# Kernel tuning notes

Hardware: AMD Instinct MI355X
Metric: run time of the kernel (lower is better)

Reference implementation:

```python
import jax, jax.numpy as jnp
import numpy as np

N_NODES = 50000
N_EDGES = 800000
NFEAT = 128
NHID = 64
NLAYER = 3
BN_EPS = 1e-5


def _bn(h, gamma, beta):
    # BatchNorm1d, training-mode batch statistics (biased variance)
    mu = jnp.mean(h, axis=0)
    var = jnp.mean((h - mu) ** 2, axis=0)
    return gamma * (h - mu) * jax.lax.rsqrt(var + BN_EPS) + beta


def setup_inputs() -> dict:
    key = jax.random.key(0)
    ks = jax.random.split(key, 8)
    x = jax.random.normal(ks[0], (N_NODES, NFEAT), dtype=jnp.float32)
    edge_index = jax.random.randint(ks[1], (2, N_EDGES), 0, N_NODES, dtype=jnp.int64)
    # transform: Linear(nfeat, nhid) with bias, then BN
    W_t = jax.random.normal(ks[2], (NFEAT, NHID), dtype=jnp.float32) / np.sqrt(NFEAT)
    b_t = jnp.zeros((NHID,), dtype=jnp.float32)
    g_t = jnp.ones((NHID,), dtype=jnp.float32)
    bb_t = jnp.zeros((NHID,), dtype=jnp.float32)
    # per-layer GIN MLPs (bias=False) and BN affine params, stacked over layers
    W1 = jax.random.normal(ks[3], (NLAYER, NHID, NHID), dtype=jnp.float32) / np.sqrt(NHID)
    W2 = jax.random.normal(ks[4], (NLAYER, NHID, NHID), dtype=jnp.float32) / np.sqrt(NHID)
    gamma = jnp.ones((NLAYER, NHID), dtype=jnp.float32)
    beta = jnp.zeros((NLAYER, NHID), dtype=jnp.float32)
    return {"x": x, "edge_index": edge_index, "W_t": W_t, "b_t": b_t,
            "g_t": g_t, "bb_t": bb_t, "W1": W1, "W2": W2,
            "gamma": gamma, "beta": beta}


def reference(x, edge_index, W_t, b_t, g_t, bb_t, W1, W2, gamma, beta):
    src, dst = edge_index[0], edge_index[1]
    # input transform: Linear + BN
    h = _bn(x @ W_t + b_t, g_t, bb_t)
    for i in range(NLAYER):
        # dropout p=0 -> identity
        # GINConv (eps=0): (1+eps)*h + sum_{j->i} h_j, then 2-layer MLP
        agg = h + jax.ops.segment_sum(h[src], dst, num_segments=N_NODES)
        h = jax.nn.relu(agg @ W1[i]) @ W2[i]
        h = jax.nn.relu(h)
        h = _bn(h, gamma[i], beta[i])
    # per-graph boolean-mask split is a pure partition of rows; return full matrix
    return h
```

## Files before the change

kernel.cpp:

```cpp
#include <hip/hip_runtime.h>

#define NND 50000
#define NED 800000
#define NF  128
#define NH  64
#define BN_EPS 1e-5
#define NCOPY 8
#define SCB  256
#define NSB  ((NND + SCB - 1) / SCB)
#define XNODES (NND / 8)
#define FCH  196
#define NT   782
#define PGRID (FCH * 8)
#define NE4  (NED / 4)

#define WS_HB     0
#define WS_AGG    6400000
#define WS_STATS  12800000
#define WS_DEG    (WS_STATS + 4*NCOPY*128*4)
#define WS_OFFS   (WS_DEG + NND*4)
#define WS_CUR    (WS_OFFS + (NND+4)*4)
#define WS_PARTS  (WS_CUR + NND*4)
#define WS_ESRC   (WS_PARTS + 256*4)

__device__ __forceinline__ unsigned bfrn(float x) {
    unsigned u = __float_as_uint(x);
    return (u + 0x7fffu + ((u >> 16) & 1u)) >> 16;
}
__device__ __forceinline__ unsigned pk(float lo, float hi) {
    return bfrn(lo) | (bfrn(hi) << 16);
}
__device__ __forceinline__ float ulo(unsigned u) { return __uint_as_float(u << 16); }
__device__ __forceinline__ float uhi(unsigned u) { return __uint_as_float(u & 0xffff0000u); }
__device__ __forceinline__ void upadd(unsigned u, float& lo, float& hi) {
    lo += ulo(u); hi += uhi(u);
}

__device__ __forceinline__ void bn_derive(const float* __restrict__ st, int c,
                                          const float* __restrict__ g,
                                          const float* __restrict__ b,
                                          float& sc, float& sh) {
    float sum = 0.f, ssq = 0.f;
#pragma unroll
    for (int cp = 0; cp < NCOPY; ++cp) {
        sum += st[cp * 128 + c];
        ssq += st[cp * 128 + 64 + c];
    }
    double mu  = (double)sum / (double)NND;
    double var = (double)ssq / (double)NND - mu * mu;
    if (var < 0.0) var = 0.0;
    double rs = 1.0 / sqrt(var + BN_EPS);
    double scd = (double)g[c] * rs;
    sc = (float)scd;
    sh = (float)((double)b[c] - mu * scd);
}

__global__ __launch_bounds__(256) void k_dtf(const int* __restrict__ dst,
                                             int* __restrict__ deg,
                                             const float* __restrict__ x,
                                             const float* __restrict__ Wt,
                                             const float* __restrict__ bt,
                                             unsigned* __restrict__ hB,
                                             float* __restrict__ stats) {
    __shared__ __align__(16) unsigned Wlu[NF * NH / 2];
    __shared__ __align__(16) float sT[64 * 68];
    int tid = threadIdx.x;

    if (blockIdx.x >= NT) {
        int dbid = blockIdx.x - NT;
        int xcd = dbid & 7;
        int chunk = dbid >> 3;
        int lo = xcd * XNODES;
        const int4* d4 = (const int4*)dst;
        int4 d[4];
#pragma unroll
        for (int r = 0; r < 4; ++r) {
            int i = chunk * 1024 + r * 256 + tid;
            int ii = i < NE4 ? i : NE4 - 1;
            d[r] = d4[ii];
            if (i >= NE4) d[r] = make_int4(-1, -1, -1, -1);
        }
#pragma unroll
        for (int r = 0; r < 4; ++r) {
            if ((unsigned)(d[r].x - lo) < XNODES) atomicAdd(&deg[d[r].x], 1);
            if ((unsigned)(d[r].y - lo) < XNODES) atomicAdd(&deg[d[r].y], 1);
            if ((unsigned)(d[r].z - lo) < XNODES) atomicAdd(&deg[d[r].z], 1);
            if ((unsigned)(d[r].w - lo) < XNODES) atomicAdd(&deg[d[r].w], 1);
        }
        return;
    }

    int tile = blockIdx.x;
    int base = tile * 64;
    const float4* x4 = (const float4*)x;

#pragma unroll
    for (int r = 0; r < 8; ++r) {
        int i4 = r * 256 + tid;
        float4 w = ((const float4*)Wt)[i4];
        uint2 wp; wp.x = pk(w.x, w.y); wp.y = pk(w.z, w.w);
        ((uint2*)Wlu)[i4] = wp;
    }

    int wave = tid >> 6, lane = tid & 63;
    int ti = lane & 7, tj = lane >> 3;
    int cw = wave * 32 + tj * 4;

    float acc[8][4];
#pragma unroll
    for (int i = 0; i < 8; ++i)
#pragma unroll
        for (int j = 0; j < 4; ++j) acc[i][j] = 0.f;

    for (int ch = 0; ch < 2; ++ch) {
        __syncthreads();
        float4 pf[4];
#pragma unroll
        for (int s = 0; s < 4; ++s) {
            int flat = s * 256 + tid;
            int nl = flat >> 4, q = flat & 15;
            pf[s] = make_float4(0.f, 0.f, 0.f, 0.f);
            if (base + nl < NND) pf[s] = x4[(size_t)(base + nl) * 32 + ch * 16 + q];
        }
#pragma unroll
        for (int s = 0; s < 4; ++s) {
            int flat = s * 256 + tid;
            int nl = flat >> 4, q = flat & 15;
            sT[(q * 4 + 0) * 68 + nl] = pf[s].x;
            sT[(q * 4 + 1) * 68 + nl] = pf[s].y;
            sT[(q * 4 + 2) * 68 + nl] = pf[s].z;
            sT[(q * 4 + 3) * 68 + nl] = pf[s].w;
        }
        __syncthreads();
        if (tid < 128) {
#pragma unroll 4
            for (int k = 0; k < 64; ++k) {
                const float* ap = &sT[k * 68 + ti * 8];
                float4 alo = *(const float4*)ap;
                float4 ahi = *(const float4*)(ap + 4);
                uint2 wu = *(const uint2*)&Wlu[(ch * 64 + k) * 32 + (cw >> 1)];
                float a8[8] = {alo.x, alo.y, alo.z, alo.w, ahi.x, ahi.y, ahi.z, ahi.w};
                float w4[4] = {ulo(wu.x), uhi(wu.x), ulo(wu.y), uhi(wu.y)};
#pragma unroll
                for (int i = 0; i < 8; ++i)
#pragma unroll
                    for (int j = 0; j < 4; ++j) acc[i][j] += a8[i] * w4[j];
            }
        }
    }
    if (tid >= 128) return;

    float4 bv = *(const float4*)&bt[cw];
    float bj[4] = {bv.x, bv.y, bv.z, bv.w};

    float s4[4] = {0.f, 0.f, 0.f, 0.f}, q4[4] = {0.f, 0.f, 0.f, 0.f};
    uint2* hB2 = (uint2*)hB;
#pragma unroll
    for (int i = 0; i < 8; ++i) {
        int n = base + ti * 8 + i;
        if (n < NND) {
            float o[4];
#pragma unroll
            for (int j = 0; j < 4; ++j) {
                o[j] = acc[i][j] + bj[j];
                s4[j] += o[j];
                q4[j] += o[j] * o[j];
            }
            uint2 ov; ov.x = pk(o[0], o[1]); ov.y = pk(o[2], o[3]);
            hB2[(size_t)n * 16 + wave * 8 + tj] = ov;
        }
    }
#pragma unroll
    for (int m = 1; m < 8; m <<= 1) {
#pragma unroll
        for (int j = 0; j < 4; ++j) {
            s4[j] += __shfl_xor(s4[j], m);
            q4[j] += __shfl_xor(q4[j], m);
        }
    }
    if (ti == 0) {
        int slot = (tile & (NCOPY - 1)) * 128;
#pragma unroll
        for (int j = 0; j < 4; ++j) {
            atomicAdd(&stats[slot + cw + j], s4[j]);
            atomicAdd(&stats[slot + 64 + cw + j], q4[j]);
        }
    }
}

__global__ __launch_bounds__(256) void k_fill(const int* __restrict__ src,
                                              const int* __restrict__ dst,
                                              int* __restrict__ cur,
                                              int* __restrict__ esrc) {
    int xcd = blockIdx.x & 7;
    int chunk = blockIdx.x >> 3;
    int lo = xcd * XNODES;
    const int4* d4 = (const int4*)dst;
    const int4* s4 = (const int4*)src;
    int4 d[4], s[4];
#pragma unroll
    for (int r = 0; r < 4; ++r) {
        int i = chunk * 1024 + r * 256 + threadIdx.x;
        int ii = i < NE4 ? i : NE4 - 1;
        d[r] = d4[ii];
        s[r] = s4[ii];
        if (i >= NE4) d[r] = make_int4(-1, -1, -1, -1);
    }
#pragma unroll
    for (int r = 0; r < 4; ++r) {
        if ((unsigned)(d[r].x - lo) < XNODES) esrc[atomicAdd(&cur[d[r].x], 1)] = s[r].x;
        if ((unsigned)(d[r].y - lo) < XNODES) esrc[atomicAdd(&cur[d[r].y], 1)] = s[r].y;
        if ((unsigned)(d[r].z - lo) < XNODES) esrc[atomicAdd(&cur[d[r].z], 1)] = s[r].z;
        if ((unsigned)(d[r].w - lo) < XNODES) esrc[atomicAdd(&cur[d[r].w], 1)] = s[r].w;
    }
}

__global__ __launch_bounds__(SCB) void k_part(const int* __restrict__ deg,
                                              int* __restrict__ offs,
                                              int* __restrict__ parts) {
    __shared__ int sd[SCB];
    int t = threadIdx.x;
    int i = blockIdx.x * SCB + t;
    int v = (i < NND) ? deg[i] : 0;
    sd[t] = v;
    __syncthreads();
#pragma unroll
    for (int off = 1; off < SCB; off <<= 1) {
        int u = (t >= off) ? sd[t - off] : 0;
        __syncthreads();
        sd[t] += u;
        __syncthreads();
    }
    if (i < NND) offs[i] = sd[t] - v;
    if (t == SCB - 1) parts[blockIdx.x] = sd[t];
}

__global__ __launch_bounds__(256) void k_apply(int* __restrict__ offs,
                                               const int* __restrict__ parts,
                                               int* __restrict__ cur) {
    __shared__ int sd[256];
    int t = threadIdx.x;
    int v = (t < NSB) ? parts[t] : 0;
    sd[t] = v;
    __syncthreads();
#pragma unroll
    for (int off = 1; off < 256; off <<= 1) {
        int u = (t >= off) ? sd[t - off] : 0;
        __syncthreads();
        sd[t] += u;
        __syncthreads();
    }
    int c = blockIdx.x;
    int add = sd[c] - parts[c];
    int i = blockIdx.x * 256 + t;
    if (i < NND) {
        int o = offs[i] + add;
        offs[i] = o;
        cur[i] = o;
    }
    if (i == NND) offs[NND] = NED;
}

__global__ __launch_bounds__(256) void k_agg(const uint4* __restrict__ hB4,
                                             uint4* __restrict__ aggB4,
                                             const float* __restrict__ stats,
                                             const float* __restrict__ g,
                                             const float* __restrict__ b,
                                             const int* __restrict__ offs,
                                             const int* __restrict__ esrc) {
    int tid  = threadIdx.x;
    int lane = tid & 63;
    int wv   = tid >> 6;
    int n = blockIdx.x * 4 + wv;
    int q = lane & 7;
    int r = lane >> 3;

    float scl, shl;
    bn_derive(stats, lane, g, b, scl, shl);

    int e0 = offs[n], e1 = offs[n + 1];
    int deg = e1 - e0;

    float a[8];
#pragma unroll
    for (int i = 0; i < 8; ++i) a[i] = 0.f;

    if (r == 0) {
        uint4 u = hB4[(size_t)n * 8 + q];
        upadd(u.x, a[0], a[1]); upadd(u.y, a[2], a[3]);
        upadd(u.z, a[4], a[5]); upadd(u.w, a[6], a[7]);
    }

    for (int bb = e0; bb < e1; bb += 64) {
        int m = e1 - bb; if (m > 64) m = 64;
        int idx = (lane < m) ? esrc[bb + lane] : 0;
        int ng = (m + 7) >> 3;
        uint4 u[8];
#pragma unroll
        for (int gI = 0; gI < 8; ++gI) {
            if (gI < ng) {
                int e = gI * 8 + r;
                int j = __shfl(idx, e & 63);
                u[gI] = make_uint4(0u, 0u, 0u, 0u);
                if (e < m) u[gI] = hB4[(size_t)j * 8 + q];
            }
        }
#pragma unroll
        for (int gI = 0; gI < 8; ++gI) {
            if (gI < ng) {
                upadd(u[gI].x, a[0], a[1]); upadd(u[gI].y, a[2], a[3]);
                upadd(u[gI].z, a[4], a[5]); upadd(u[gI].w, a[6], a[7]);
            }
        }
    }

#pragma unroll
    for (int msk = 8; msk <= 32; msk <<= 1)
#pragma unroll
        for (int i = 0; i < 8; ++i) a[i] += __shfl_xor(a[i], msk);

    float sc8[8], sh8[8];
#pragma unroll
    for (int j = 0; j < 8; ++j) {
        sc8[j] = __shfl(scl, q * 8 + j);
        sh8[j] = __shfl(shl, q * 8 + j);
    }

    if (r == 0) {
        float dn = (float)(deg + 1);
        float o[8];
#pragma unroll
        for (int j = 0; j < 8; ++j) o[j] = sc8[j] * a[j] + dn * sh8[j];
        uint4 ov;
        ov.x = pk(o[0], o[1]); ov.y = pk(o[2], o[3]);
        ov.z = pk(o[4], o[5]); ov.w = pk(o[6], o[7]);
        aggB4[(size_t)n * 8 + q] = ov;
    }
}

__global__ __launch_bounds__(128) void k_mlp(const uint4* __restrict__ aggB4,
                                             float* __restrict__ outF,
                                             unsigned* __restrict__ hBo,
                                             float* __restrict__ stats,
                                             const float* __restrict__ W1,
                                             const float* __restrict__ W2) {
    __shared__ __align__(16) float W1l[NH * NH];
    __shared__ __align__(16) float W2l[NH * NH];
    __shared__ __align__(16) float sT[64 * 68];
    int tid  = threadIdx.x;
    int wave = tid >> 6, lane = tid & 63;
    int ti = lane & 7, tj = lane >> 3;
    int tile = blockIdx.x;
    int base = tile * 64;
    int cw = wave * 32 + tj * 4;

#pragma unroll
    for (int r = 0; r < 8; ++r) {
        int i4 = r * 128 + tid;
        ((float4*)W1l)[i4] = ((const float4*)W1)[i4];
        ((float4*)W2l)[i4] = ((const float4*)W2)[i4];
    }
#pragma unroll
    for (int s = 0; s < 4; ++s) {
        int i4 = s * 128 + tid;
        int nl = i4 >> 3, q = i4 & 7;
        uint4 u = make_uint4(0u, 0u, 0u, 0u);
        if (base + nl < NND) u = aggB4[(size_t)(base + nl) * 8 + q];
        sT[(q * 8 + 0) * 68 + nl] = ulo(u.x);
        sT[(q * 8 + 1) * 68 + nl] = uhi(u.x);
        sT[(q * 8 + 2) * 68 + nl] = ulo(u.y);
        sT[(q * 8 + 3) * 68 + nl] = uhi(u.y);
        sT[(q * 8 + 4) * 68 + nl] = ulo(u.z);
        sT[(q * 8 + 5) * 68 + nl] = uhi(u.z);
        sT[(q * 8 + 6) * 68 + nl] = ulo(u.w);
        sT[(q * 8 + 7) * 68 + nl] = uhi(u.w);
    }
    __syncthreads();

    float a1[8][4];
#pragma unroll
    for (int i = 0; i < 8; ++i)
#pragma unroll
        for (int j = 0; j < 4; ++j) a1[i][j] = 0.f;
#pragma unroll 4
    for (int k = 0; k < 64; ++k) {
        const float* ap = &sT[k * 68 + ti * 8];
        float4 alo = *(const float4*)ap;
        float4 ahi = *(const float4*)(ap + 4);
        float4 wv  = *(const float4*)&W1l[k * NH + cw];
        float a8[8] = {alo.x, alo.y, alo.z, alo.w, ahi.x, ahi.y, ahi.z, ahi.w};
        float w4[4] = {wv.x, wv.y, wv.z, wv.w};
#pragma unroll
        for (int i = 0; i < 8; ++i)
#pragma unroll
            for (int j = 0; j < 4; ++j) a1[i][j] += a8[i] * w4[j];
    }
#pragma unroll
    for (int i = 0; i < 8; ++i)
#pragma unroll
        for (int j = 0; j < 4; ++j) a1[i][j] = fmaxf(a1[i][j], 0.f);

    __syncthreads();
#pragma unroll
    for (int j = 0; j < 4; ++j) {
        float* p = &sT[(cw + j) * 68 + ti * 8];
        float4 lo = {a1[0][j], a1[1][j], a1[2][j], a1[3][j]};
        float4 hi = {a1[4][j], a1[5][j], a1[6][j], a1[7][j]};
        *(float4*)p = lo;
        *(float4*)(p + 4) = hi;
    }
    __syncthreads();

    float a2[8][4];
#pragma unroll
    for (int i = 0; i < 8; ++i)
#pragma unroll
        for (int j = 0; j < 4; ++j) a2[i][j] = 0.f;
#pragma unroll 4
    for (int k = 0; k < 64; ++k) {
        const float* ap = &sT[k * 68 + ti * 8];
        float4 alo = *(const float4*)ap;
        float4 ahi = *(const float4*)(ap + 4);
        float4 wv  = *(const float4*)&W2l[k * NH + cw];
        float a8[8] = {alo.x, alo.y, alo.z, alo.w, ahi.x, ahi.y, ahi.z, ahi.w};
        float w4[4] = {wv.x, wv.y, wv.z, wv.w};
#pragma unroll
        for (int i = 0; i < 8; ++i)
#pragma unroll
            for (int j = 0; j < 4; ++j) a2[i][j] += a8[i] * w4[j];
    }

    float s4[4] = {0.f, 0.f, 0.f, 0.f}, q4[4] = {0.f, 0.f, 0.f, 0.f};
    uint2* hBo2 = (uint2*)hBo;
#pragma unroll
    for (int i = 0; i < 8; ++i) {
        int n = base + ti * 8 + i;
        if (n < NND) {
            float o[4];
#pragma unroll
            for (int j = 0; j < 4; ++j) {
                o[j] = fmaxf(a2[i][j], 0.f);
                s4[j] += o[j];
                q4[j] += o[j] * o[j];
            }
            if (outF) *(float4*)&outF[(size_t)n * NH + cw] = *(float4*)&o[0];
            if (hBo) {
                uint2 ov; ov.x = pk(o[0], o[1]); ov.y = pk(o[2], o[3]);
                hBo2[(size_t)n * 16 + wave * 8 + tj] = ov;
            }
        }
    }
#pragma unroll
    for (int m = 1; m < 8; m <<= 1) {
#pragma unroll
        for (int j = 0; j < 4; ++j) {
            s4[j] += __shfl_xor(s4[j], m);
            q4[j] += __shfl_xor(q4[j], m);
        }
    }
    if (ti == 0) {
        int slot = (tile & (NCOPY - 1)) * 128;
#pragma unroll
        for (int j = 0; j < 4; ++j) {
            atomicAdd(&stats[slot + cw + j], s4[j]);
            atomicAdd(&stats[slot + 64 + cw + j], q4[j]);
        }
    }
}

__global__ __launch_bounds__(256) void k_bnout(float* __restrict__ h,
                                               const float* __restrict__ stats,
                                               const float* __restrict__ g,
                                               const float* __restrict__ b) {
    __shared__ float sl[128];
    int tid = threadIdx.x;
    if (tid < 64) {
        float sc, sh;
        bn_derive(stats, tid, g, b, sc, sh);
        sl[tid]      = sc;
        sl[64 + tid] = sh;
    }
    __syncthreads();
    int i4 = blockIdx.x * 256 + tid;
    if (i4 < NND * NH / 4) {
        int cg = i4 & 15;
        float4 v   = ((float4*)h)[i4];
        float4 scv = *(float4*)&sl[cg * 4];
        float4 shv = *(float4*)&sl[64 + cg * 4];
        v.x = v.x * scv.x + shv.x;
        v.y = v.y * scv.y + shv.y;
        v.z = v.z * scv.z + shv.z;
        v.w = v.w * scv.w + shv.w;
        ((float4*)h)[i4] = v;
    }
}

extern "C" void kernel_launch(void* const* d_in, const int* in_sizes, int n_in,
                              void* d_out, int out_size, void* d_ws, size_t ws_size,
                              hipStream_t stream) {
    const float* x     = (const float*)d_in[0];
    const int*   ei    = (const int*)d_in[1];
    const float* Wt    = (const float*)d_in[2];
    const float* bt    = (const float*)d_in[3];
    const float* gt    = (const float*)d_in[4];
    const float* bbt   = (const float*)d_in[5];
    const float* W1    = (const float*)d_in[6];
    const float* W2    = (const float*)d_in[7];
    const float* gamma = (const float*)d_in[8];
    const float* beta  = (const float*)d_in[9];
    float* out = (float*)d_out;

    char* ws = (char*)d_ws;
    unsigned* hB    = (unsigned*)(ws + WS_HB);
    unsigned* aggB  = (unsigned*)(ws + WS_AGG);
    float*    stats = (float*)(ws + WS_STATS);
    int*      deg   = (int*)(ws + WS_DEG);
    int*      offs  = (int*)(ws + WS_OFFS);
    int*      cur   = (int*)(ws + WS_CUR);
    int*      parts = (int*)(ws + WS_PARTS);
    int*      esrc  = (int*)(ws + WS_ESRC);

    float* st0 = stats;
    float* st1 = stats + NCOPY * 128;
    float* st2 = stats + 2 * NCOPY * 128;
    float* st3 = stats + 3 * NCOPY * 128;

    const int* srcv = ei;
    const int* dstv = ei + NED;

    hipMemsetAsync(stats, 0, 4 * NCOPY * 128 * 4 + NND * 4, stream);

    k_dtf<<<NT + PGRID, 256, 0, stream>>>(dstv, deg, x, Wt, bt, hB, st0);
    k_part<<<NSB, SCB, 0, stream>>>(deg, offs, parts);
    k_apply<<<NSB, 256, 0, stream>>>(offs, parts, cur);
    k_fill<<<PGRID, 256, 0, stream>>>(srcv, dstv, cur, esrc);

    const int NB = NND / 4;

    k_agg<<<NB, 256, 0, stream>>>((const uint4*)hB, (uint4*)aggB, st0, gt, bbt, offs, esrc);
    k_mlp<<<NT, 128, 0, stream>>>((const uint4*)aggB, nullptr, hB, st1, W1, W2);

    k_agg<<<NB, 256, 0, stream>>>((const uint4*)hB, (uint4*)aggB, st1, gamma, beta, offs, esrc);
    k_mlp<<<NT, 128, 0, stream>>>((const uint4*)aggB, nullptr, hB, st2, W1 + 4096, W2 + 4096);

    k_agg<<<NB, 256, 0, stream>>>((const uint4*)hB, (uint4*)aggB, st2, gamma + 64, beta + 64, offs, esrc);
    k_mlp<<<NT, 128, 0, stream>>>((const uint4*)aggB, out, nullptr, st3, W1 + 8192, W2 + 8192);

    k_bnout<<<(NND * NH / 4 + 255) / 256, 256, 0, stream>>>(out, st3, gamma + 128, beta + 128);
}
```

Measured before the change: 311.3 us.

## Partition each node's CSR neighbor list by source half for gather locality

Counts, per destination, how many in-edges come from sources in the lower half of the node range. Each node's edge slots are split into a low-source segment and a high-source segment through two fill cursors. The aggregation kernel walks the low segment and then the high segment. The aim is better cache locality in the bf16 feature gathers, since concurrent waves tend to touch the same half of the feature table. The cost is an extra atomic degree counter, an extra cursor array, and a second gather loop with more partial tail batches per node.

```diff
diff --git a/kernel.cpp b/kernel.cpp
--- a/kernel.cpp
+++ b/kernel.cpp
@@ -13,14 +13,17 @@
 #define NT   782
 #define PGRID (FCH * 8)
 #define NE4  (NED / 4)
+#define NLOW (NND / 2)
 
 #define WS_HB     0
 #define WS_AGG    6400000
 #define WS_STATS  12800000
 #define WS_DEG    (WS_STATS + 4*NCOPY*128*4)
-#define WS_OFFS   (WS_DEG + NND*4)
+#define WS_LDEG   (WS_DEG + NND*4)
+#define WS_OFFS   (WS_LDEG + NND*4)
 #define WS_CUR    (WS_OFFS + (NND+4)*4)
-#define WS_PARTS  (WS_CUR + NND*4)
+#define WS_CURB   (WS_CUR + NND*4)
+#define WS_PARTS  (WS_CURB + NND*4)
 #define WS_ESRC   (WS_PARTS + 256*4)
 
 __device__ __forceinline__ unsigned bfrn(float x) {
@@ -55,8 +58,38 @@
     sh = (float)((double)b[c] - mu * scd);
 }
 
-__global__ __launch_bounds__(256) void k_dtf(const int* __restrict__ dst,
+__device__ __forceinline__ void gather_range(const uint4* __restrict__ hB4,
+                                             const int* __restrict__ esrc,
+                                             int from, int to,
+                                             int lane, int q, int r, float a[8]) {
+    for (int bb = from; bb < to; bb += 64) {
+        int m = to - bb; if (m > 64) m = 64;
+        int idx = (lane < m) ? esrc[bb + lane] : 0;
+        int ng = (m + 7) >> 3;
+        uint4 u[8];
+#pragma unroll
+        for (int gI = 0; gI < 8; ++gI) {
+            if (gI < ng) {
+                int e = gI * 8 + r;
+                int j = __shfl(idx, e & 63);
+                u[gI] = make_uint4(0u, 0u, 0u, 0u);
+                if (e < m) u[gI] = hB4[(size_t)j * 8 + q];
+            }
+        }
+#pragma unroll
+        for (int gI = 0; gI < 8; ++gI) {
+            if (gI < ng) {
+                upadd(u[gI].x, a[0], a[1]); upadd(u[gI].y, a[2], a[3]);
+                upadd(u[gI].z, a[4], a[5]); upadd(u[gI].w, a[6], a[7]);
+            }
+        }
+    }
+}
+
+__global__ __launch_bounds__(256) void k_dtf(const int* __restrict__ src,
+                                             const int* __restrict__ dst,
                                              int* __restrict__ deg,
+                                             int* __restrict__ ldeg,
                                              const float* __restrict__ x,
                                              const float* __restrict__ Wt,
                                              const float* __restrict__ bt,
@@ -72,20 +105,34 @@
         int chunk = dbid >> 3;
         int lo = xcd * XNODES;
         const int4* d4 = (const int4*)dst;
-        int4 d[4];
+        const int4* s4 = (const int4*)src;
+        int4 d[4], s[4];
 #pragma unroll
         for (int r = 0; r < 4; ++r) {
             int i = chunk * 1024 + r * 256 + tid;
             int ii = i < NE4 ? i : NE4 - 1;
             d[r] = d4[ii];
+            s[r] = s4[ii];
             if (i >= NE4) d[r] = make_int4(-1, -1, -1, -1);
         }
 #pragma unroll
         for (int r = 0; r < 4; ++r) {
-            if ((unsigned)(d[r].x - lo) < XNODES) atomicAdd(&deg[d[r].x], 1);
-            if ((unsigned)(d[r].y - lo) < XNODES) atomicAdd(&deg[d[r].y], 1);
-            if ((unsigned)(d[r].z - lo) < XNODES) atomicAdd(&deg[d[r].z], 1);
-            if ((unsigned)(d[r].w - lo) < XNODES) atomicAdd(&deg[d[r].w], 1);
+            if ((unsigned)(d[r].x - lo) < XNODES) {
+                atomicAdd(&deg[d[r].x], 1);
+                if ((unsigned)s[r].x < NLOW) atomicAdd(&ldeg[d[r].x], 1);
+            }
+            if ((unsigned)(d[r].y - lo) < XNODES) {
+                atomicAdd(&deg[d[r].y], 1);
+                if ((unsigned)s[r].y < NLOW) atomicAdd(&ldeg[d[r].y], 1);
+            }
+            if ((unsigned)(d[r].z - lo) < XNODES) {
+                atomicAdd(&deg[d[r].z], 1);
+                if ((unsigned)s[r].z < NLOW) atomicAdd(&ldeg[d[r].z], 1);
+            }
+            if ((unsigned)(d[r].w - lo) < XNODES) {
+                atomicAdd(&deg[d[r].w], 1);
+                if ((unsigned)s[r].w < NLOW) atomicAdd(&ldeg[d[r].w], 1);
+            }
         }
         return;
     }
@@ -190,7 +237,8 @@
 
 __global__ __launch_bounds__(256) void k_fill(const int* __restrict__ src,
                                               const int* __restrict__ dst,
-                                              int* __restrict__ cur,
+                                              int* __restrict__ curA,
+                                              int* __restrict__ curB,
                                               int* __restrict__ esrc) {
     int xcd = blockIdx.x & 7;
     int chunk = blockIdx.x >> 3;
@@ -208,10 +256,22 @@
     }
 #pragma unroll
     for (int r = 0; r < 4; ++r) {
-        if ((unsigned)(d[r].x - lo) < XNODES) esrc[atomicAdd(&cur[d[r].x], 1)] = s[r].x;
-        if ((unsigned)(d[r].y - lo) < XNODES) esrc[atomicAdd(&cur[d[r].y], 1)] = s[r].y;
-        if ((unsigned)(d[r].z - lo) < XNODES) esrc[atomicAdd(&cur[d[r].z], 1)] = s[r].z;
-        if ((unsigned)(d[r].w - lo) < XNODES) esrc[atomicAdd(&cur[d[r].w], 1)] = s[r].w;
+        if ((unsigned)(d[r].x - lo) < XNODES) {
+            int* c = ((unsigned)s[r].x < NLOW) ? curA : curB;
+            esrc[atomicAdd(&c[d[r].x], 1)] = s[r].x;
+        }
+        if ((unsigned)(d[r].y - lo) < XNODES) {
+            int* c = ((unsigned)s[r].y < NLOW) ? curA : curB;
+            esrc[atomicAdd(&c[d[r].y], 1)] = s[r].y;
+        }
+        if ((unsigned)(d[r].z - lo) < XNODES) {
+            int* c = ((unsigned)s[r].z < NLOW) ? curA : curB;
+            esrc[atomicAdd(&c[d[r].z], 1)] = s[r].z;
+        }
+        if ((unsigned)(d[r].w - lo) < XNODES) {
+            int* c = ((unsigned)s[r].w < NLOW) ? curA : curB;
+            esrc[atomicAdd(&c[d[r].w], 1)] = s[r].w;
+        }
     }
 }
 
@@ -237,7 +297,9 @@
 
 __global__ __launch_bounds__(256) void k_apply(int* __restrict__ offs,
                                                const int* __restrict__ parts,
-                                               int* __restrict__ cur) {
+                                               const int* __restrict__ ldeg,
+                                               int* __restrict__ curA,
+                                               int* __restrict__ curB) {
     __shared__ int sd[256];
     int t = threadIdx.x;
     int v = (t < NSB) ? parts[t] : 0;
@@ -256,7 +318,8 @@
     if (i < NND) {
         int o = offs[i] + add;
         offs[i] = o;
-        cur[i] = o;
+        curA[i] = o;
+        curB[i] = o + ldeg[i];
     }
     if (i == NND) offs[NND] = NED;
 }
@@ -267,6 +330,7 @@
                                              const float* __restrict__ g,
                                              const float* __restrict__ b,
                                              const int* __restrict__ offs,
+                                             const int* __restrict__ ldeg,
                                              const int* __restrict__ esrc) {
     int tid  = threadIdx.x;
     int lane = tid & 63;
@@ -278,8 +342,9 @@
     float scl, shl;
     bn_derive(stats, lane, g, b, scl, shl);
 
-    int e0 = offs[n], e1 = offs[n + 1];
-    int deg = e1 - e0;
+    int e0 = offs[n], e2 = offs[n + 1];
+    int e1 = e0 + ldeg[n];
+    int deg = e2 - e0;
 
     float a[8];
 #pragma unroll
@@ -291,28 +356,8 @@
         upadd(u.z, a[4], a[5]); upadd(u.w, a[6], a[7]);
     }
 
-    for (int bb = e0; bb < e1; bb += 64) {
-        int m = e1 - bb; if (m > 64) m = 64;
-        int idx = (lane < m) ? esrc[bb + lane] : 0;
-        int ng = (m + 7) >> 3;
-        uint4 u[8];
-#pragma unroll
-        for (int gI = 0; gI < 8; ++gI) {
-            if (gI < ng) {
-                int e = gI * 8 + r;
-                int j = __shfl(idx, e & 63);
-                u[gI] = make_uint4(0u, 0u, 0u, 0u);
-                if (e < m) u[gI] = hB4[(size_t)j * 8 + q];
-            }
-        }
-#pragma unroll
-        for (int gI = 0; gI < 8; ++gI) {
-            if (gI < ng) {
-                upadd(u[gI].x, a[0], a[1]); upadd(u[gI].y, a[2], a[3]);
-                upadd(u[gI].z, a[4], a[5]); upadd(u[gI].w, a[6], a[7]);
-            }
-        }
-    }
+    gather_range(hB4, esrc, e0, e1, lane, q, r, a);
+    gather_range(hB4, esrc, e1, e2, lane, q, r, a);
 
 #pragma unroll
     for (int msk = 8; msk <= 32; msk <<= 1)
@@ -515,8 +560,10 @@
     unsigned* aggB  = (unsigned*)(ws + WS_AGG);
     float*    stats = (float*)(ws + WS_STATS);
     int*      deg   = (int*)(ws + WS_DEG);
+    int*      ldeg  = (int*)(ws + WS_LDEG);
     int*      offs  = (int*)(ws + WS_OFFS);
-    int*      cur   = (int*)(ws + WS_CUR);
+    int*      curA  = (int*)(ws + WS_CUR);
+    int*      curB  = (int*)(ws + WS_CURB);
     int*      parts = (int*)(ws + WS_PARTS);
     int*      esrc  = (int*)(ws + WS_ESRC);
 
@@ -528,22 +575,22 @@
     const int* srcv = ei;
     const int* dstv = ei + NED;
 
-    hipMemsetAsync(stats, 0, 4 * NCOPY * 128 * 4 + NND * 4, stream);
-
-    k_dtf<<<NT + PGRID, 256, 0, stream>>>(dstv, deg, x, Wt, bt, hB, st0);
+    hipMemsetAsync(stats, 0, 4 * NCOPY * 128 * 4 + 2 * NND * 4, stream);
+
+    k_dtf<<<NT + PGRID, 256, 0, stream>>>(srcv, dstv, deg, ldeg, x, Wt, bt, hB, st0);
     k_part<<<NSB, SCB, 0, stream>>>(deg, offs, parts);
-    k_apply<<<NSB, 256, 0, stream>>>(offs, parts, cur);
-    k_fill<<<PGRID, 256, 0, stream>>>(srcv, dstv, cur, esrc);
+    k_apply<<<NSB, 256, 0, stream>>>(offs, parts, ldeg, curA, curB);
+    k_fill<<<PGRID, 256, 0, stream>>>(srcv, dstv, curA, curB, esrc);
 
     const int NB = NND / 4;
 
-    k_agg<<<NB, 256, 0, stream>>>((const uint4*)hB, (uint4*)aggB, st0, gt, bbt, offs, esrc);
+    k_agg<<<NB, 256, 0, stream>>>((const uint4*)hB, (uint4*)aggB, st0, gt, bbt, offs, ldeg, esrc);
     k_mlp<<<NT, 128, 0, stream>>>((const uint4*)aggB, nullptr, hB, st1, W1, W2);
 
-    k_agg<<<NB, 256, 0, stream>>>((const uint4*)hB, (uint4*)aggB, st1, gamma, beta, offs, esrc);
+    k_agg<<<NB, 256, 0, stream>>>((const uint4*)hB, (uint4*)aggB, st1, gamma, beta, offs, ldeg, esrc);
     k_mlp<<<NT, 128, 0, stream>>>((const uint4*)aggB, nullptr, hB, st2, W1 + 4096, W2 + 4096);
 
-    k_agg<<<NB, 256, 0, stream>>>((const uint4*)hB, (uint4*)aggB, st2, gamma + 64, beta + 64, offs, esrc);
+    k_agg<<<NB, 256, 0, stream>>>((const uint4*)hB, (uint4*)aggB, st2, gamma + 64, beta + 64, offs, ldeg, esrc);
     k_mlp<<<NT, 128, 0, stream>>>((const uint4*)aggB, out, nullptr, st3, W1 + 8192, W2 + 8192);
 
     k_bnout<<<(NND * NH / 4 + 255) / 256, 256, 0, stream>>>(out, st3, gamma + 128, beta + 128);
```

Result: slower. 347.9 us (+11.7%).

## Split bf16 feature storage into two column-half planes and aggregate per half

Applied to the files above, without the earlier changes.

Node features are stored as two separate planes of 32 columns each instead of interleaved 64-column rows, and the gather-aggregation kernel is launched twice, once per half. Each pass's random gather working set becomes half the size (50000×64B), which improves L2 hit rate for irregular neighbor reads. The cost is twice the launches, re-reading the edge index and offsets in both passes, and narrower 64-byte gathers per edge.

```diff
diff --git a/kernel.cpp b/kernel.cpp
--- a/kernel.cpp
+++ b/kernel.cpp
@@ -167,7 +167,7 @@
                 q4[j] += o[j] * o[j];
             }
             uint2 ov; ov.x = pk(o[0], o[1]); ov.y = pk(o[2], o[3]);
-            hB2[(size_t)n * 16 + wave * 8 + tj] = ov;
+            hB2[((size_t)wave * NND + n) * 8 + tj] = ov;
         }
     }
 #pragma unroll
@@ -267,16 +267,18 @@
                                              const float* __restrict__ g,
                                              const float* __restrict__ b,
                                              const int* __restrict__ offs,
-                                             const int* __restrict__ esrc) {
+                                             const int* __restrict__ esrc,
+                                             int half) {
     int tid  = threadIdx.x;
     int lane = tid & 63;
     int wv   = tid >> 6;
     int n = blockIdx.x * 4 + wv;
-    int q = lane & 7;
-    int r = lane >> 3;
+    int q = lane & 3;
+    int r = lane >> 2;
+    size_t hbase = (size_t)half * NND;
 
     float scl, shl;
-    bn_derive(stats, lane, g, b, scl, shl);
+    bn_derive(stats, half * 32 + (lane & 31), g, b, scl, shl);
 
     int e0 = offs[n], e1 = offs[n + 1];
     int deg = e1 - e0;
@@ -286,7 +288,7 @@
     for (int i = 0; i < 8; ++i) a[i] = 0.f;
 
     if (r == 0) {
-        uint4 u = hB4[(size_t)n * 8 + q];
+        uint4 u = hB4[(hbase + n) * 4 + q];
         upadd(u.x, a[0], a[1]); upadd(u.y, a[2], a[3]);
         upadd(u.z, a[4], a[5]); upadd(u.w, a[6], a[7]);
     }
@@ -294,19 +296,19 @@
     for (int bb = e0; bb < e1; bb += 64) {
         int m = e1 - bb; if (m > 64) m = 64;
         int idx = (lane < m) ? esrc[bb + lane] : 0;
-        int ng = (m + 7) >> 3;
-        uint4 u[8];
-#pragma unroll
-        for (int gI = 0; gI < 8; ++gI) {
+        int ng = (m + 15) >> 4;
+        uint4 u[4];
+#pragma unroll
+        for (int gI = 0; gI < 4; ++gI) {
             if (gI < ng) {
-                int e = gI * 8 + r;
+                int e = gI * 16 + r;
                 int j = __shfl(idx, e & 63);
                 u[gI] = make_uint4(0u, 0u, 0u, 0u);
-                if (e < m) u[gI] = hB4[(size_t)j * 8 + q];
+                if (e < m) u[gI] = hB4[(hbase + j) * 4 + q];
             }
         }
 #pragma unroll
-        for (int gI = 0; gI < 8; ++gI) {
+        for (int gI = 0; gI < 4; ++gI) {
             if (gI < ng) {
                 upadd(u[gI].x, a[0], a[1]); upadd(u[gI].y, a[2], a[3]);
                 upadd(u[gI].z, a[4], a[5]); upadd(u[gI].w, a[6], a[7]);
@@ -315,7 +317,7 @@
     }
 
 #pragma unroll
-    for (int msk = 8; msk <= 32; msk <<= 1)
+    for (int msk = 4; msk <= 32; msk <<= 1)
 #pragma unroll
         for (int i = 0; i < 8; ++i) a[i] += __shfl_xor(a[i], msk);
 
@@ -334,7 +336,7 @@
         uint4 ov;
         ov.x = pk(o[0], o[1]); ov.y = pk(o[2], o[3]);
         ov.z = pk(o[4], o[5]); ov.w = pk(o[6], o[7]);
-        aggB4[(size_t)n * 8 + q] = ov;
+        aggB4[(hbase + n) * 4 + q] = ov;
     }
 }
 
@@ -363,17 +365,19 @@
 #pragma unroll
     for (int s = 0; s < 4; ++s) {
         int i4 = s * 128 + tid;
-        int nl = i4 >> 3, q = i4 & 7;
+        int nl = i4 >> 3, z = i4 & 7;
+        int h = z >> 2, qq = z & 3;
         uint4 u = make_uint4(0u, 0u, 0u, 0u);
-        if (base + nl < NND) u = aggB4[(size_t)(base + nl) * 8 + q];
-        sT[(q * 8 + 0) * 68 + nl] = ulo(u.x);
-        sT[(q * 8 + 1) * 68 + nl] = uhi(u.x);
-        sT[(q * 8 + 2) * 68 + nl] = ulo(u.y);
-        sT[(q * 8 + 3) * 68 + nl] = uhi(u.y);
-        sT[(q * 8 + 4) * 68 + nl] = ulo(u.z);
-        sT[(q * 8 + 5) * 68 + nl] = uhi(u.z);
-        sT[(q * 8 + 6) * 68 + nl] = ulo(u.w);
-        sT[(q * 8 + 7) * 68 + nl] = uhi(u.w);
+        if (base + nl < NND) u = aggB4[((size_t)h * NND + base + nl) * 4 + qq];
+        int c0 = h * 32 + qq * 8;
+        sT[(c0 + 0) * 68 + nl] = ulo(u.x);
+        sT[(c0 + 1) * 68 + nl] = uhi(u.x);
+        sT[(c0 + 2) * 68 + nl] = ulo(u.y);
+        sT[(c0 + 3) * 68 + nl] = uhi(u.y);
+        sT[(c0 + 4) * 68 + nl] = ulo(u.z);
+        sT[(c0 + 5) * 68 + nl] = uhi(u.z);
+        sT[(c0 + 6) * 68 + nl] = ulo(u.w);
+        sT[(c0 + 7) * 68 + nl] = uhi(u.w);
     }
     __syncthreads();
 
@@ -446,7 +450,7 @@
             if (outF) *(float4*)&outF[(size_t)n * NH + cw] = *(float4*)&o[0];
             if (hBo) {
                 uint2 ov; ov.x = pk(o[0], o[1]); ov.y = pk(o[2], o[3]);
-                hBo2[(size_t)n * 16 + wave * 8 + tj] = ov;
+                hBo2[((size_t)wave * NND + n) * 8 + tj] = ov;
             }
         }
     }
@@ -537,13 +541,16 @@
 
     const int NB = NND / 4;
 
-    k_agg<<<NB, 256, 0, stream>>>((const uint4*)hB, (uint4*)aggB, st0, gt, bbt, offs, esrc);
+    k_agg<<<NB, 256, 0, stream>>>((const uint4*)hB, (uint4*)aggB, st0, gt, bbt, offs, esrc, 0);
+    k_agg<<<NB, 256, 0, stream>>>((const uint4*)hB, (uint4*)aggB, st0, gt, bbt, offs, esrc, 1);
     k_mlp<<<NT, 128, 0, stream>>>((const uint4*)aggB, nullptr, hB, st1, W1, W2);
 
-    k_agg<<<NB, 256, 0, stream>>>((const uint4*)hB, (uint4*)aggB, st1, gamma, beta, offs, esrc);
+    k_agg<<<NB, 256, 0, stream>>>((const uint4*)hB, (uint4*)aggB, st1, gamma, beta, offs, esrc, 0);
+    k_agg<<<NB, 256, 0, stream>>>((const uint4*)hB, (uint4*)aggB, st1, gamma, beta, offs, esrc, 1);
     k_mlp<<<NT, 128, 0, stream>>>((const uint4*)aggB, nullptr, hB, st2, W1 + 4096, W2 + 4096);
 
-    k_agg<<<NB, 256, 0, stream>>>((const uint4*)hB, (uint4*)aggB, st2, gamma + 64, beta + 64, offs, esrc);
+    k_agg<<<NB, 256, 0, stream>>>((const uint4*)hB, (uint4*)aggB, st2, gamma + 64, beta + 64, offs, esrc, 0);
+    k_agg<<<NB, 256, 0, stream>>>((const uint4*)hB, (uint4*)aggB, st2, gamma + 64, beta + 64, offs, esrc, 1);
     k_mlp<<<NT, 128, 0, stream>>>((const uint4*)aggB, out, nullptr, st3, W1 + 8192, W2 + 8192);
 
     k_bnout<<<(NND * NH / 4 + 255) / 256, 256, 0, stream>>>(out, st3, gamma + 128, beta + 128);
```

After: 382.4 us. 22.8% more time.
